# Optimization experiments

Hardware: AMD Instinct MI355X
Metric: run time of the kernel (lower is better)

## Reference

```python
import jax, jax.numpy as jnp
import numpy as np

B, S, D = 32, 1024, 1280          # batch, spatial tokens, hidden_size
CROSS = 768                        # cross_attention_dim
HEADS = 20
HD = D // HEADS                    # 64
N_AOE, N_IMG = 16, 16              # disease / anatomy token counts
SCALE = 1.0 / float(np.sqrt(HD))


def _split_heads(x):
    # [B, N, D] -> [B, H, N, HD]
    b, n, _ = x.shape
    return x.reshape(b, n, HEADS, HD).transpose(0, 2, 1, 3)


def _attend(q, k, v):
    # q: [B,H,S,HD], k/v: [B,H,K,HD]  (K is tiny, 16)
    scores = jnp.einsum('bhsd,bhkd->bhsk', q, k) * SCALE
    probs = jax.nn.softmax(scores, axis=-1)
    return jnp.einsum('bhsk,bhkd->bhsd', probs, v)


def setup_inputs() -> dict:
    key = jax.random.key(0)
    ks = jax.random.split(key, 10)
    g = lambda k, shape, sc=0.02: jax.random.normal(k, shape, jnp.float32) * sc
    return {
        'hidden_states': jax.random.normal(ks[0], (B, S, D), jnp.float32),
        'encoder_hidden_states': jax.random.normal(ks[1], (B, N_AOE + N_IMG + 16, CROSS), jnp.float32),
        'w_q': g(ks[2], (D, D)),            # attn.to_q, bias=False
        'w_k': g(ks[3], (D, CROSS)),        # attn.to_k (anatomy branch)
        'w_v': g(ks[4], (D, CROSS)),        # attn.to_v
        'w_k_dis': g(ks[5], (D, CROSS)),    # self.to_k_dis
        'w_v_dis': g(ks[6], (D, CROSS)),    # self.to_v_dis
        'w_gate': g(ks[7], (1, CROSS)),     # gate_modulator (randomized to exercise path; init is zeros)
        'b_gate': jnp.zeros((1,), jnp.float32),
        'anat_gate_logit': jnp.float32(0.0),  # logit(0.5) for block_type='both'
        'dis_gate_logit': jnp.float32(0.0),
        'w_out': g(ks[8], (D, D)),          # attn.to_out[0]
        'b_out': jnp.zeros((D,), jnp.float32),
    }


def reference(hidden_states, encoder_hidden_states, w_q, w_k, w_v, w_k_dis,
              w_v_dis, w_gate, b_gate, anat_gate_logit, dis_gate_logit,
              w_out, b_out):
    residual = hidden_states
    b = hidden_states.shape[0]

    # token splits (delta path disabled: delta_scale == 0.0)
    dis_tokens = encoder_hidden_states[:, :N_AOE, :]
    anat_tokens = encoder_hidden_states[:, N_AOE:N_AOE + N_IMG, :]

    # projections (torch Linear: x @ W^T)
    query = _split_heads(hidden_states @ w_q.T)          # [B,H,S,HD]
    k_anat = _split_heads(anat_tokens @ w_k.T)           # [B,H,16,HD]
    v_anat = _split_heads(anat_tokens @ w_v.T)
    k_dis = _split_heads(dis_tokens @ w_k_dis.T)
    v_dis = _split_heads(dis_tokens @ w_v_dis.T)

    z_anat = _attend(query, k_anat, v_anat)              # [B,H,S,HD]
    z_dis = _attend(query, k_dis, v_dis)

    # severity-driven gate shift
    severity = dis_tokens.mean(axis=1)                   # [B, CROSS]
    shift = (severity @ w_gate.T + b_gate).reshape(b, 1, 1, 1)
    anat_gate = jax.nn.sigmoid(anat_gate_logit - shift)
    dis_gate = jax.nn.sigmoid(dis_gate_logit + shift)

    z_final = anat_gate * z_anat + dis_gate * z_dis      # [B,H,S,HD]

    out = z_final.transpose(0, 2, 1, 3).reshape(b, -1, D)
    out = out @ w_out.T + b_out                          # to_out[0]; to_out[1] is dropout (eval identity)
    out = out + residual                                 # residual_connection=True, rescale_output_factor=1.0
    return out
```

## Files before the change

kernel.cpp:

```cpp
#include <hip/hip_runtime.h>
#include <stdint.h>

#define B_     32
#define S_     1024
#define D_     1280
#define CROSS_ 768
#define NTOK   16
#define SCALE_ 0.125f

typedef __bf16 bf16x8 __attribute__((ext_vector_type(8)));
typedef float  f32x4  __attribute__((ext_vector_type(4)));
typedef unsigned short ushort_t;
typedef unsigned int   uint_t;

__device__ __forceinline__ float b2f(ushort_t h){ return __uint_as_float(((uint_t)h)<<16); }
__device__ __forceinline__ ushort_t f2b(float f){
  uint_t u = __float_as_uint(f);
  u += 0x7FFFu + ((u>>16)&1u);
  return (ushort_t)(u>>16);
}
__device__ __forceinline__ uint_t pk2(float x, float y){
  return (uint_t)f2b(x) | ((uint_t)f2b(y)<<16);
}

__device__ __forceinline__ void gload_lds16(const void* g, void* l){
  __builtin_amdgcn_global_load_lds((const __attribute__((address_space(1))) void*)g,
                                   (__attribute__((address_space(3))) void*)l, 16, 0, 0);
}

struct CvtArgs { const float* src[7]; ushort_t* dst[7]; int n[7]; };
__global__ void cvt_kernel(CvtArgs a){
  int t = blockIdx.y;
  const float* s = a.src[t]; ushort_t* d = a.dst[t]; int n = a.n[t];
  int i = (blockIdx.x*blockDim.x + threadIdx.x)*4;
  if(i >= n) return;
  float4 v = *(const float4*)(s+i);
  uint2 o; o.x = pk2(v.x,v.y); o.y = pk2(v.z,v.w);
  *(uint2*)(d+i) = o;
}

__global__ void cvt_big(const float* __restrict__ s, ushort_t* __restrict__ d, int n){
  int i = (blockIdx.x*blockDim.x + threadIdx.x)*8;
  if(i >= n) return;
  float4 v0 = *(const float4*)(s+i), v1 = *(const float4*)(s+i+4);
  uint4 o = { pk2(v0.x,v0.y), pk2(v0.z,v0.w), pk2(v1.x,v1.y), pk2(v1.z,v1.w) };
  *(uint4*)(d+i) = o;
}

__global__ void gates_kernel(const float* __restrict__ enc,
                             const float* __restrict__ w_gate,
                             const float* __restrict__ b_gate,
                             const float* __restrict__ aLog,
                             const float* __restrict__ dLog,
                             float* __restrict__ gates){
  int b = blockIdx.x, tid = threadIdx.x;
  __shared__ float red[256];
  float acc = 0.f;
  for(int k = tid; k < CROSS_; k += 256){
    float s = 0.f;
    for(int t = 0; t < NTOK; ++t)
      s += enc[(size_t)(b*48 + t)*CROSS_ + k];
    acc += w_gate[k] * s;
  }
  red[tid] = acc; __syncthreads();
  for(int off = 128; off > 0; off >>= 1){
    if(tid < off) red[tid] += red[tid+off];
    __syncthreads();
  }
  if(tid == 0){
    float shift = red[0]*(1.f/16.f) + b_gate[0];
    gates[b*2+0] = 1.f/(1.f+__expf(shift - aLog[0]));
    gates[b*2+1] = 1.f/(1.f+__expf(-(dLog[0] + shift)));
  }
}

__global__ __launch_bounds__(256) void kv_gemm(const ushort_t* __restrict__ enc,
      const ushort_t* __restrict__ wk,  const ushort_t* __restrict__ wv,
      const ushort_t* __restrict__ wkd, const ushort_t* __restrict__ wvd,
      ushort_t* __restrict__ kv){
  __shared__ __align__(16) ushort_t As[128*64];
  __shared__ __align__(16) ushort_t Bs[128*64];
  const int tau = blockIdx.z;
  const ushort_t* W = (tau==0)? wk : (tau==1)? wv : (tau==2)? wkd : wvd;
  const int tok_off = (tau < 2) ? NTOK : 0;
  const int m0 = blockIdx.x*128, n0 = blockIdx.y*128;
  const int tid = threadIdx.x, l = tid & 63, w = tid >> 6;
  const int wm = (w&1)*64, wn = (w>>1)*64;
  const f32x4 fz = {0.f,0.f,0.f,0.f};
  f32x4 acc[4][4];
  #pragma unroll
  for(int i=0;i<4;++i){
    #pragma unroll
    for(int j=0;j<4;++j) acc[i][j] = fz;
  }
  for(int kt = 0; kt < CROSS_/64; ++kt){
    const int k0 = kt*64;
    #pragma unroll
    for(int i=0;i<4;++i){
      int row = (w*4+i)*8 + (l>>3);
      int c   = l & 7;
      int gm  = m0 + row;
      int er  = (gm>>4)*48 + tok_off + (gm&15);
      gload_lds16(enc + (size_t)er*CROSS_ + k0 + c*8, As + (w*4+i)*512);
      gload_lds16(W  + (size_t)(n0+row)*CROSS_ + k0 + c*8, Bs + (w*4+i)*512);
    }
    __syncthreads();
    #pragma unroll
    for(int ks = 0; ks < 64; ks += 32){
      bf16x8 a[4], bq[4];
      #pragma unroll
      for(int i=0;i<4;++i) a[i]  = *(const bf16x8*)&As[(wm+i*16+(l&15))*64 + ks + (l>>4)*8];
      #pragma unroll
      for(int j=0;j<4;++j) bq[j] = *(const bf16x8*)&Bs[(wn+j*16+(l&15))*64 + ks + (l>>4)*8];
      #pragma unroll
      for(int i=0;i<4;++i){
        #pragma unroll
        for(int j=0;j<4;++j)
          acc[i][j] = __builtin_amdgcn_mfma_f32_16x16x32_bf16(a[i], bq[j], acc[i][j], 0,0,0);
      }
    }
    __syncthreads();
  }
  #pragma unroll
  for(int i=0;i<4;++i){
    #pragma unroll
    for(int j=0;j<4;++j){
      #pragma unroll
      for(int r=0;r<4;++r){
        int m = m0 + wm + i*16 + (l>>4)*4 + r;
        int n = n0 + wn + j*16 + (l&15);
        int b = m >> 4, t = m & 15;
        kv[(((size_t)tau*B_ + b)*NTOK + t)*D_ + n] = f2b(acc[i][j][r]);
      }
    }
  }
}

#define VMW(n)  asm volatile("s_waitcnt vmcnt(" #n ")" ::: "memory")
#define FENCE() asm volatile("" ::: "memory")
#define BARX()  do{ FENCE(); __builtin_amdgcn_s_barrier(); FENCE(); }while(0)
#define LGKM0() asm volatile("s_waitcnt lgkmcnt(0)" ::: "memory")

__device__ __forceinline__ void stage_aq(const ushort_t* __restrict__ g,
                                         ushort_t* le, int tid){
  int row = tid >> 3;
  int c   = ((tid & 7) ^ (row & 7)) << 3;
  gload_lds16(g + (size_t)row*D_ + c, le + (tid>>6)*512);
}
__device__ __forceinline__ void stage_b2(const ushort_t* __restrict__ g,
                                         ushort_t* lh, int s0, int tid){
  int w   = tid >> 6;
  int blk = w >> 2;
  int t   = tid & 255;
  int rr  = s0 + blk*64 + (t >> 3);
  int c   = ((t & 7) ^ (rr & 7)) << 3;
  gload_lds16(g + (size_t)rr*D_ + c, lh + (s0 + blk*64)*64 + (w&3)*512);
}

#define A3(s) (lds + (s)*16384)
#define B2(u) (lds + 49152 + (u)*16384)
#define ST_GA0(tt,s) { stage_aq(Asrc + (size_t)  0*D_ + (tt)*64, A3(s),          tid); \
                       stage_aq(Asrc + (size_t)128*D_ + (tt)*64, A3(s) + 8192,   tid); }
#define ST_GA1(tt,s) { stage_aq(Asrc + (size_t) 64*D_ + (tt)*64, A3(s) + 4096,   tid); \
                       stage_aq(Asrc + (size_t)192*D_ + (tt)*64, A3(s) + 12288,  tid); }
#define ST_GB0(tt,u) { stage_b2(Bsrc + (size_t)  0*D_ + (tt)*64, B2(u),        0, tid); \
                       stage_b2(Bsrc + (size_t)128*D_ + (tt)*64, B2(u) + 8192, 0, tid); }
#define ST_GB1(tt,u) { stage_b2(Bsrc + (size_t)  0*D_ + (tt)*64, B2(u),       32, tid); \
                       stage_b2(Bsrc + (size_t)128*D_ + (tt)*64, B2(u) + 8192,32, tid); }
#define DS_A(qi, Ab) { _Pragma("unroll") for(int i=0;i<4;++i){ \
      a[i][0] = *(const bf16x8*)&(Ab)[((qi)*64 + i*16 + lr)*64 + csw0]; \
      a[i][1] = *(const bf16x8*)&(Ab)[((qi)*64 + i*16 + lr)*64 + csw1]; } }
#define DS_B(qj, Bb) { _Pragma("unroll") for(int j=0;j<2;++j){ \
      bb[j][0] = *(const bf16x8*)&(Bb)[(bro + ((qj)*2+j)*16)*64 + csw0]; \
      bb[j][1] = *(const bf16x8*)&(Bb)[(bro + ((qj)*2+j)*16)*64 + csw1]; } }
#define MM(qi,qj) { __builtin_amdgcn_s_setprio(1); \
    _Pragma("unroll") for(int i=0;i<4;++i){ _Pragma("unroll") for(int j=0;j<2;++j){ \
      acc[(qi)*4+i][(qj)*2+j] = __builtin_amdgcn_mfma_f32_16x16x32_bf16(a[i][0], bb[j][0], acc[(qi)*4+i][(qj)*2+j],0,0,0); \
      acc[(qi)*4+i][(qj)*2+j] = __builtin_amdgcn_mfma_f32_16x16x32_bf16(a[i][1], bb[j][1], acc[(qi)*4+i][(qj)*2+j],0,0,0); } } \
    __builtin_amdgcn_s_setprio(0); }

#define TILE_N(t, s_cur, s_pf2, u_cur, u_nx) { \
    const ushort_t* Ab = A3(s_cur) + wr*8192; \
    const ushort_t* Bb = B2(u_cur) + (wc>>1)*8192; \
    DS_A(0,Ab); DS_B(0,Bb); ST_GB0((t)+1,u_nx); VMW(6); BARX(); MM(0,0); BARX(); \
    DS_B(1,Bb);             ST_GB1((t)+1,u_nx);         BARX(); MM(0,1); BARX(); \
    DS_A(1,Ab); DS_B(0,Bb); ST_GA0((t)+2,s_pf2);        BARX(); MM(1,0); BARX(); \
    DS_B(1,Bb);             ST_GA1((t)+2,s_pf2); VMW(6); BARX(); MM(1,1); BARX(); }

#define MAINLOOP4 \
  ST_GA0(0,0); ST_GA1(0,0); ST_GB0(0,0); ST_GB1(0,0); ST_GA0(1,1); ST_GA1(1,1); \
  VMW(6); \
  BARX(); \
  for(int tt6 = 0; tt6 < 18; tt6 += 6){ \
    _Pragma("unroll") \
    for(int uu = 0; uu < 6; ++uu){ \
      TILE_N(tt6+uu, (uu%3), ((uu+2)%3), (uu&1), ((uu+1)&1)); \
    } \
  } \
  {  \
    const ushort_t* Ab = A3(0) + wr*8192; \
    const ushort_t* Bb = B2(0) + (wc>>1)*8192; \
    DS_A(0,Ab); DS_B(0,Bb); ST_GB0(19,1); VMW(6); BARX(); MM(0,0); BARX(); \
    DS_B(1,Bb);             ST_GB1(19,1);         BARX(); MM(0,1); BARX(); \
    DS_A(1,Ab); DS_B(0,Bb);                       BARX(); MM(1,0); BARX(); \
    DS_B(1,Bb);                           VMW(2); BARX(); MM(1,1); BARX(); \
  } \
  {  \
    const ushort_t* Ab = A3(1) + wr*8192; \
    const ushort_t* Bb = B2(1) + (wc>>1)*8192; \
    DS_A(0,Ab); DS_B(0,Bb); VMW(0); BARX(); MM(0,0); BARX(); \
    DS_B(1,Bb);                     BARX(); MM(0,1); BARX(); \
    DS_A(1,Ab); DS_B(0,Bb);         BARX(); MM(1,0); BARX(); \
    DS_B(1,Bb);                             MM(1,1); \
  }

__global__ __launch_bounds__(512,2) void gemm1_attn_8p(
      const ushort_t* __restrict__ X, const ushort_t* __restrict__ Wq,
      const ushort_t* __restrict__ kv, const float* __restrict__ gates,
      ushort_t* __restrict__ Z){
  __shared__ __align__(16) ushort_t lds[81920];
  const int lid = (blockIdx.x & 7)*80 + (blockIdx.x >> 3);
  const int m0 = (lid/5)*256, n0 = (lid%5)*256;
  const int tid = threadIdx.x, l = tid & 63, w = tid >> 6;
  const int wr = w >> 2, wc = w & 3;
  const int lr = l & 15;
  const int csw0 = ((l>>4)*8)    ^ ((l&7)<<3);
  const int csw1 = (32+(l>>4)*8) ^ ((l&7)<<3);
  const int bro  = (wc & 1)*64 + lr;
  const ushort_t* Asrc = X  + (size_t)m0*D_;
  const ushort_t* Bsrc = Wq + (size_t)n0*D_;
  const f32x4 fz = {0.f,0.f,0.f,0.f};
  f32x4 acc[8][4];
  #pragma unroll
  for(int i=0;i<8;++i){
    #pragma unroll
    for(int j=0;j<4;++j) acc[i][j] = fz;
  }
  bf16x8 a[4][2], bb[2][2];

  MAINLOOP4

  BARX();
  const int b = m0 >> 10;
  const float gA = gates[b*2+0], gD = gates[b*2+1];
  ushort_t* R = lds + w*8192;
  const ushort_t* kbase = kv + ((size_t)b*NTOK + lr)*D_ + n0 + wc*64 + (l>>4)*8;
  bf16x8 kA0 = *(const bf16x8*)(kbase);
  bf16x8 kA1 = *(const bf16x8*)(kbase + 32);
  bf16x8 kD0 = *(const bf16x8*)(kbase + (size_t)2*B_*NTOK*D_);
  bf16x8 kD1 = *(const bf16x8*)(kbase + (size_t)2*B_*NTOK*D_ + 32);
  f32x4 scA[8], scD[8];
  #pragma unroll
  for(int i=0;i<8;++i){ scA[i] = fz; scD[i] = fz; }
  #pragma unroll
  for(int i=0;i<8;++i){
    ushort_t* qs = R + (i&1)*1024;
    #pragma unroll
    for(int j=0;j<4;++j){
      #pragma unroll
      for(int r=0;r<4;++r){
        int row = (l>>4)*4 + r;
        int col = j*16 + lr;
        qs[row*64 + ((((col>>3) ^ (row&7))<<3) | (col&7))] = f2b(acc[i][j][r]);
      }
    }
    LGKM0();
    bf16x8 af0 = *(const bf16x8*)&qs[lr*64 + ((((l>>4))   ^ (lr&7))<<3)];
    bf16x8 af1 = *(const bf16x8*)&qs[lr*64 + (((4+(l>>4)) ^ (lr&7))<<3)];
    scA[i] = __builtin_amdgcn_mfma_f32_16x16x32_bf16(af0, kA0, scA[i], 0,0,0);
    scA[i] = __builtin_amdgcn_mfma_f32_16x16x32_bf16(af1, kA1, scA[i], 0,0,0);
    scD[i] = __builtin_amdgcn_mfma_f32_16x16x32_bf16(af0, kD0, scD[i], 0,0,0);
    scD[i] = __builtin_amdgcn_mfma_f32_16x16x32_bf16(af1, kD1, scD[i], 0,0,0);
  }
  uint4 vld[4];
  #pragma unroll
  for(int it=0; it<4; ++it){
    int u = it*64 + l;
    int tp = u >> 3, c = u & 7;
    int tensor = (tp < 16) ? 1 : 3;
    int t = tp & 15;
    vld[it] = *(const uint4*)(kv + (((size_t)tensor*B_ + b)*NTOK + t)*D_
                                 + n0 + wc*64 + c*8);
  }
  LGKM0();
  #pragma unroll
  for(int i=0;i<8;++i){
    #pragma unroll
    for(int r=0;r<4;++r){
      float vA = scA[i][r]*SCALE_, vD = scD[i][r]*SCALE_;
      float mA = vA, mD = vD;
      #pragma unroll
      for(int off=1; off<16; off<<=1){
        mA = fmaxf(mA, __shfl_xor(mA, off));
        mD = fmaxf(mD, __shfl_xor(mD, off));
      }
      float eA = __expf(vA - mA), eD = __expf(vD - mD);
      float sA = eA, sD = eD;
      #pragma unroll
      for(int off=1; off<16; off<<=1){
        sA += __shfl_xor(sA, off);
        sD += __shfl_xor(sD, off);
      }
      int lrow = i*16 + (l>>4)*4 + r;
      R[lrow*44 + lr]      = f2b(gA*eA/sA);
      R[lrow*44 + 16 + lr] = f2b(gD*eD/sD);
    }
  }
  ushort_t* vts = R + 5632;
  #pragma unroll
  for(int it=0; it<4; ++it){
    int u = it*64 + l;
    int tp = u >> 3, c = u & 7;
    const ushort_t* pv = (const ushort_t*)&vld[it];
    #pragma unroll
    for(int e=0;e<8;++e) vts[(c*8+e)*40 + tp] = pv[e];
  }
  LGKM0();
  bf16x8 pa[8], vb[4];
  #pragma unroll
  for(int i=0;i<8;++i) pa[i] = *(const bf16x8*)&R[(i*16+lr)*44 + (l>>4)*8];
  #pragma unroll
  for(int j=0;j<4;++j)  vb[j] = *(const bf16x8*)&vts[(j*16+lr)*40 + (l>>4)*8];
  f32x4 z[8][4];
  #pragma unroll
  for(int i=0;i<8;++i){
    #pragma unroll
    for(int j=0;j<4;++j)
      z[i][j] = __builtin_amdgcn_mfma_f32_16x16x32_bf16(pa[i], vb[j], fz, 0,0,0);
  }
  #pragma unroll
  for(int i=0;i<8;++i){
    #pragma unroll
    for(int j=0;j<4;++j){
      #pragma unroll
      for(int r=0;r<4;++r){
        int row = m0 + wr*128 + i*16 + (l>>4)*4 + r;
        int col = n0 + wc*64 + j*16 + lr;
        Z[(size_t)row*D_ + col] = f2b(z[i][j][r]);
      }
    }
  }
}

__global__ __launch_bounds__(512,2) void gemm2_8p(
      const ushort_t* __restrict__ Zin, const ushort_t* __restrict__ Wo,
      const float* __restrict__ bias, const float* __restrict__ resid,
      float* __restrict__ out){
  __shared__ __align__(16) ushort_t lds[81920];
  const int lid = (blockIdx.x & 7)*80 + (blockIdx.x >> 3);
  const int m0 = (lid/5)*256, n0 = (lid%5)*256;
  const int tid = threadIdx.x, l = tid & 63, w = tid >> 6;
  const int wr = w >> 2, wc = w & 3;
  const int lr = l & 15;
  const int csw0 = ((l>>4)*8)    ^ ((l&7)<<3);
  const int csw1 = (32+(l>>4)*8) ^ ((l&7)<<3);
  const int bro  = (wc & 1)*64 + lr;
  const ushort_t* Asrc = Zin + (size_t)m0*D_;
  const ushort_t* Bsrc = Wo  + (size_t)n0*D_;
  const f32x4 fz = {0.f,0.f,0.f,0.f};
  f32x4 acc[8][4];
  #pragma unroll
  for(int i=0;i<8;++i){
    #pragma unroll
    for(int j=0;j<4;++j) acc[i][j] = fz;
  }
  bf16x8 a[4][2], bb[2][2];

  MAINLOOP4

  float bj[4];
  #pragma unroll
  for(int j=0;j<4;++j) bj[j] = bias[n0 + wc*64 + j*16 + lr];
  #pragma unroll
  for(int i=0;i<8;++i){
    #pragma unroll
    for(int j=0;j<4;++j){
      #pragma unroll
      for(int r=0;r<4;++r){
        int m = m0 + wr*128 + i*16 + (l>>4)*4 + r;
        int n = n0 + wc*64 + j*16 + lr;
        out[(size_t)m*D_ + n] = acc[i][j][r] + bj[j] + resid[(size_t)m*D_ + n];
      }
    }
  }
}

extern "C" void kernel_launch(void* const* d_in, const int* in_sizes, int n_in,
                              void* d_out, int out_size, void* d_ws, size_t ws_size,
                              hipStream_t stream){
  const float* hidden = (const float*)d_in[0];
  const float* enc    = (const float*)d_in[1];
  const float* w_q    = (const float*)d_in[2];
  const float* w_k    = (const float*)d_in[3];
  const float* w_v    = (const float*)d_in[4];
  const float* w_kd   = (const float*)d_in[5];
  const float* w_vd   = (const float*)d_in[6];
  const float* w_gate = (const float*)d_in[7];
  const float* b_gate = (const float*)d_in[8];
  const float* aLog   = (const float*)d_in[9];
  const float* dLog   = (const float*)d_in[10];
  const float* w_out  = (const float*)d_in[11];
  const float* b_out  = (const float*)d_in[12];
  float* out = (float*)d_out;

  char* ws = (char*)d_ws;
  ushort_t* z_bf   = (ushort_t*)(ws + 0);
  ushort_t* kv_bf  = (ushort_t*)(ws + 83886080);
  ushort_t* wq_bf  = (ushort_t*)(ws + 89128960);
  ushort_t* wk_bf  = (ushort_t*)(ws + 92405760);
  ushort_t* wv_bf  = (ushort_t*)(ws + 94371840);
  ushort_t* wkd_bf = (ushort_t*)(ws + 96337920);
  ushort_t* wvd_bf = (ushort_t*)(ws + 98304000);
  ushort_t* wo_bf  = (ushort_t*)(ws + 100270080);
  ushort_t* enc_bf = (ushort_t*)(ws + 103546880);
  float*    gates  = (float*)   (ws + 105906176);

  ushort_t* hid_bf = (ushort_t*)d_out;

  CvtArgs ca;
  ca.src[0]=w_q;   ca.dst[0]=wq_bf;  ca.n[0]=D_*D_;
  ca.src[1]=w_k;   ca.dst[1]=wk_bf;  ca.n[1]=D_*CROSS_;
  ca.src[2]=w_v;   ca.dst[2]=wv_bf;  ca.n[2]=D_*CROSS_;
  ca.src[3]=w_kd;  ca.dst[3]=wkd_bf; ca.n[3]=D_*CROSS_;
  ca.src[4]=w_vd;  ca.dst[4]=wvd_bf; ca.n[4]=D_*CROSS_;
  ca.src[5]=w_out; ca.dst[5]=wo_bf;  ca.n[5]=D_*D_;
  ca.src[6]=enc;   ca.dst[6]=enc_bf; ca.n[6]=B_*48*CROSS_;
  cvt_kernel<<<dim3(1600,7), 256, 0, stream>>>(ca);
  cvt_big<<<20480, 256, 0, stream>>>(hidden, hid_bf, B_*S_*D_);

  gates_kernel<<<32, 256, 0, stream>>>(enc, w_gate, b_gate, aLog, dLog, gates);
  kv_gemm<<<dim3(4,10,4), 256, 0, stream>>>(enc_bf, wk_bf, wv_bf, wkd_bf, wvd_bf, kv_bf);
  gemm1_attn_8p<<<640, 512, 0, stream>>>(hid_bf, wq_bf, kv_bf, gates, z_bf);
  gemm2_8p<<<640, 512, 0, stream>>>(z_bf, wo_bf, b_out, hidden, out);
}
```

Baseline: 656.6 us.

## Load full B fragment once per K-tile and halve barriers in GEMM main loop

Restructures the shared GEMM main loop used by both kernels. Each K-tile now loads all four B fragments into registers at once and runs two large MFMA groups, instead of four smaller groups split by eight barriers. This cuts B re-reads from LDS (B was reloaded for each A half), reduces the barrier count per tile from eight to two, and changes the vmcnt waits. In exchange it uses more VGPRs for B fragments under a 512x2 launch bound, which risks spills. Prefetches now have less separation from compute, so LDS buffer reuse safety depends on the remaining barriers.

```diff
diff --git a/kernel.cpp b/kernel.cpp
--- a/kernel.cpp
+++ b/kernel.cpp
@@ -170,48 +170,46 @@
 #define DS_A(qi, Ab) { _Pragma("unroll") for(int i=0;i<4;++i){ \
       a[i][0] = *(const bf16x8*)&(Ab)[((qi)*64 + i*16 + lr)*64 + csw0]; \
       a[i][1] = *(const bf16x8*)&(Ab)[((qi)*64 + i*16 + lr)*64 + csw1]; } }
-#define DS_B(qj, Bb) { _Pragma("unroll") for(int j=0;j<2;++j){ \
-      bb[j][0] = *(const bf16x8*)&(Bb)[(bro + ((qj)*2+j)*16)*64 + csw0]; \
-      bb[j][1] = *(const bf16x8*)&(Bb)[(bro + ((qj)*2+j)*16)*64 + csw1]; } }
-#define MM(qi,qj) { __builtin_amdgcn_s_setprio(1); \
-    _Pragma("unroll") for(int i=0;i<4;++i){ _Pragma("unroll") for(int j=0;j<2;++j){ \
-      acc[(qi)*4+i][(qj)*2+j] = __builtin_amdgcn_mfma_f32_16x16x32_bf16(a[i][0], bb[j][0], acc[(qi)*4+i][(qj)*2+j],0,0,0); \
-      acc[(qi)*4+i][(qj)*2+j] = __builtin_amdgcn_mfma_f32_16x16x32_bf16(a[i][1], bb[j][1], acc[(qi)*4+i][(qj)*2+j],0,0,0); } } \
+#define DS_BALL(Bb) { _Pragma("unroll") for(int jj=0;jj<4;++jj){ \
+      bball[jj][0] = *(const bf16x8*)&(Bb)[(bro + jj*16)*64 + csw0]; \
+      bball[jj][1] = *(const bf16x8*)&(Bb)[(bro + jj*16)*64 + csw1]; } }
+#define MM2(qi) { __builtin_amdgcn_s_setprio(1); \
+    _Pragma("unroll") for(int i=0;i<4;++i){ _Pragma("unroll") for(int jj=0;jj<4;++jj){ \
+      acc[(qi)*4+i][jj] = __builtin_amdgcn_mfma_f32_16x16x32_bf16(a[i][0], bball[jj][0], acc[(qi)*4+i][jj],0,0,0); \
+      acc[(qi)*4+i][jj] = __builtin_amdgcn_mfma_f32_16x16x32_bf16(a[i][1], bball[jj][1], acc[(qi)*4+i][jj],0,0,0); } } \
     __builtin_amdgcn_s_setprio(0); }
 
-#define TILE_N(t, s_cur, s_pf2, u_cur, u_nx) { \
+#define TILE_T(t, s_cur, s_pf2, u_cur, u_nx) { \
     const ushort_t* Ab = A3(s_cur) + wr*8192; \
     const ushort_t* Bb = B2(u_cur) + (wc>>1)*8192; \
-    DS_A(0,Ab); DS_B(0,Bb); ST_GB0((t)+1,u_nx); VMW(6); BARX(); MM(0,0); BARX(); \
-    DS_B(1,Bb);             ST_GB1((t)+1,u_nx);         BARX(); MM(0,1); BARX(); \
-    DS_A(1,Ab); DS_B(0,Bb); ST_GA0((t)+2,s_pf2);        BARX(); MM(1,0); BARX(); \
-    DS_B(1,Bb);             ST_GA1((t)+2,s_pf2); VMW(6); BARX(); MM(1,1); BARX(); }
-
-#define MAINLOOP4 \
-  ST_GA0(0,0); ST_GA1(0,0); ST_GB0(0,0); ST_GB1(0,0); ST_GA0(1,1); ST_GA1(1,1); \
-  VMW(6); \
+    DS_BALL(Bb); DS_A(0,Ab); ST_GB0((t)+1,u_nx); ST_GB1((t)+1,u_nx); \
+    MM2(0); BARX(); \
+    DS_A(1,Ab); ST_GA0((t)+2,s_pf2); ST_GA1((t)+2,s_pf2); \
+    MM2(1); VMW(4); BARX(); }
+
+#define MAINLOOP5 \
+  ST_GB0(0,0); ST_GB1(0,0); ST_GA0(0,0); ST_GA1(0,0); ST_GA0(1,1); ST_GA1(1,1); \
+  VMW(4); \
   BARX(); \
   for(int tt6 = 0; tt6 < 18; tt6 += 6){ \
     _Pragma("unroll") \
     for(int uu = 0; uu < 6; ++uu){ \
-      TILE_N(tt6+uu, (uu%3), ((uu+2)%3), (uu&1), ((uu+1)&1)); \
+      TILE_T(tt6+uu, (uu%3), ((uu+2)%3), (uu&1), ((uu+1)&1)); \
     } \
   } \
   {  \
     const ushort_t* Ab = A3(0) + wr*8192; \
     const ushort_t* Bb = B2(0) + (wc>>1)*8192; \
-    DS_A(0,Ab); DS_B(0,Bb); ST_GB0(19,1); VMW(6); BARX(); MM(0,0); BARX(); \
-    DS_B(1,Bb);             ST_GB1(19,1);         BARX(); MM(0,1); BARX(); \
-    DS_A(1,Ab); DS_B(0,Bb);                       BARX(); MM(1,0); BARX(); \
-    DS_B(1,Bb);                           VMW(2); BARX(); MM(1,1); BARX(); \
+    DS_BALL(Bb); DS_A(0,Ab); ST_GB0(19,1); ST_GB1(19,1); \
+    MM2(0); BARX(); \
+    DS_A(1,Ab); \
+    MM2(1); VMW(0); BARX(); \
   } \
   {  \
     const ushort_t* Ab = A3(1) + wr*8192; \
     const ushort_t* Bb = B2(1) + (wc>>1)*8192; \
-    DS_A(0,Ab); DS_B(0,Bb); VMW(0); BARX(); MM(0,0); BARX(); \
-    DS_B(1,Bb);                     BARX(); MM(0,1); BARX(); \
-    DS_A(1,Ab); DS_B(0,Bb);         BARX(); MM(1,0); BARX(); \
-    DS_B(1,Bb);                             MM(1,1); \
+    DS_BALL(Bb); DS_A(0,Ab); MM2(0); \
+    DS_A(1,Ab);              MM2(1); \
   }
 
 __global__ __launch_bounds__(512,2) void gemm1_attn_8p(
@@ -236,9 +234,9 @@
     #pragma unroll
     for(int j=0;j<4;++j) acc[i][j] = fz;
   }
-  bf16x8 a[4][2], bb[2][2];
-
-  MAINLOOP4
+  bf16x8 a[4][2], bball[4][2];
+
+  MAINLOOP5
 
   BARX();
   const int b = m0 >> 10;
@@ -364,9 +362,9 @@
     #pragma unroll
     for(int j=0;j<4;++j) acc[i][j] = fz;
   }
-  bf16x8 a[4][2], bb[2][2];
-
-  MAINLOOP4
+  bf16x8 a[4][2], bball[4][2];
+
+  MAINLOOP5
 
   float bj[4];
   #pragma unroll
```

Measured after the change: 649.0 us. Within noise of the previous version (-1.2%).
